# Performance work log

Hardware: AMD Instinct MI355X
Metric: run time of the kernel (lower is better)

## Reference

```python
import jax, jax.numpy as jnp
import numpy as np

DROPOUT_P = 0.1  # original source passed p=1 (degenerate, zeros output); 0.1 used for a meaningful baseline


def setup_inputs() -> dict:
    key0 = jax.random.key(0)
    ks = jax.random.split(key0, 11)
    B, H, L, D, DQK, DV = 2, 8, 2048, 1024, 64, 64
    return {
        "query": jax.random.normal(ks[0], (B, H, L, D), jnp.float32),
        "key":   jax.random.normal(ks[1], (B, H, L, D), jnp.float32),
        "value": jax.random.normal(ks[2], (B, H, L, D), jnp.float32),
        "Wq": jax.random.normal(ks[3], (D, DQK), jnp.float32) * (D ** -0.5),
        "bq": jax.random.normal(ks[4], (DQK,), jnp.float32) * 0.02,
        "Wk": jax.random.normal(ks[5], (D, DQK), jnp.float32) * (D ** -0.5),
        "bk": jax.random.normal(ks[6], (DQK,), jnp.float32) * 0.02,
        "Wv": jax.random.normal(ks[7], (D, DV), jnp.float32) * (D ** -0.5),
        "bv": jax.random.normal(ks[8], (DV,), jnp.float32) * 0.02,
        "Wo": jax.random.normal(ks[9], (DV, D), jnp.float32) * (DV ** -0.5),
        "bo": jax.random.normal(ks[10], (D,), jnp.float32) * 0.02,
    }


def reference(query, key, value, Wq, bq, Wk, bk, Wv, bv, Wo, bo):
    # Per-head linear projections on 4D inputs (B,H,L,d_model)
    q = query @ Wq + bq            # (B,H,Lq,dqk)
    k = key @ Wk + bk              # (B,H,Lk,dqk)
    v = value @ Wv + bv            # (B,H,Lk,dv)
    # Quirky scale from source: q.size(2)*q.size(3)/key.size(2) * key.size(-1)**-0.5
    dk = (q.shape[2] * q.shape[3] / key.shape[2]) * (key.shape[-1] ** -0.5)
    scores = jnp.einsum('bhqd,bhkd->bhqk', q, k) * jnp.float32(dk)
    attn = jax.nn.softmax(scores, axis=-1)
    # Deterministic dropout with fixed key (inverted-scale, matching F.dropout)
    keep = jax.random.bernoulli(jax.random.key(42), 1.0 - DROPOUT_P, attn.shape)
    attn = jnp.where(keep, attn / (1.0 - DROPOUT_P), jnp.float32(0.0))
    out = jnp.einsum('bhqk,bhkd->bhqd', attn, v)  # (B,H,Lq,dv)
    return out @ Wo + bo                           # (B,H,Lq,d_model)
```

## Files before the change

### kernel.cpp

```cpp
#include <hip/hip_runtime.h>
#include <stdint.h>

typedef _Float16 f16;
typedef __attribute__((ext_vector_type(8))) _Float16 f16x8;
typedef __attribute__((ext_vector_type(4))) float f32x4;

__device__ __forceinline__ uint32_t rotl1(uint32_t x, uint32_t n){
  return __builtin_amdgcn_alignbit(x, x, 32u - n);
}
__device__ __forceinline__ uint32_t tf_bits(uint32_t i){
  const uint32_t ks1 = 42u, ks2 = 0x1BD11BDAu ^ 42u;
  uint32_t x0 = 0u, x1 = i + 42u;
#define R4(a,b,c,d) \
  x0 += x1; x1 = rotl1(x1,a); x1 ^= x0; \
  x0 += x1; x1 = rotl1(x1,b); x1 ^= x0; \
  x0 += x1; x1 = rotl1(x1,c); x1 ^= x0; \
  x0 += x1; x1 = rotl1(x1,d); x1 ^= x0;
  R4(13,15,26,6)  x0 += ks1; x1 += ks2 + 1u;
  R4(17,29,16,24) x0 += ks2; x1 += 2u;
  R4(13,15,26,6)               x1 += ks1 + 3u;
  R4(17,29,16,24) x0 += ks1; x1 += ks2 + 4u;
  R4(13,15,26,6)  x0 += ks2; x1 += 5u;
#undef R4
  return x0 ^ x1;
}

template<int PACKED>
__global__ __launch_bounds__(256) void proj_kernel(
    const float* __restrict__ query, const float* __restrict__ keyp, const float* __restrict__ value,
    const float* __restrict__ Wq, const float* __restrict__ bq,
    const float* __restrict__ Wk, const float* __restrict__ bk,
    const float* __restrict__ Wv, const float* __restrict__ bv,
    const float* __restrict__ Wo,
    f16* __restrict__ qp, f16* __restrict__ kp, f16* __restrict__ vpT,
    f16* __restrict__ WoT)
{
  __shared__ __align__(16) f16 Alds[64][40];
  __shared__ __align__(16) f16 Wlds[64][40];
  const int bid = blockIdx.x;
  const int tid = threadIdx.x;
  const int lane = tid & 63, wave = tid >> 6;
  const int llo = lane & 15, lhi = lane >> 4;

  int p;
  if (PACKED == 0){
    if (bid < 256){
      int t = bid*256 + tid;
      int n = t & 1023, k = t >> 10;
      WoT[(long)n*64 + k] = (f16)Wo[(long)k*1024 + n];
      return;
    }
    p = bid - 256;
  } else {
    p = 768 + bid;
  }

  const int which = p >> 9;
  const long m0 = (long)(p & 511) * 64;
  const float* A    = which==0 ? query : (which==1 ? keyp : value);
  const float* W    = which==0 ? Wq    : (which==1 ? Wk   : Wv);
  const float* bias = which==0 ? bq    : (which==1 ? bk   : bv);

  f32x4 acc[4];
  #pragma unroll
  for (int n=0;n<4;n++){
    float bb = bias[16*n + llo];
    acc[n][0]=bb; acc[n][1]=bb; acc[n][2]=bb; acc[n][3]=bb;
  }

  const int ar = tid >> 2;
  const int ac = (tid & 3) * 8;
  const int wcol = tid & 63;
  const int wk = (tid >> 6) * 8;

  for (int k0 = 0; k0 < 1024; k0 += 32){
    {
      const float* asrc = A + (m0 + ar)*1024 + k0 + ac;
      float4 v0 = *(const float4*)asrc;
      float4 v1 = *(const float4*)(asrc + 4);
      if (PACKED == 0){
        f16* ad = &Alds[ar][ac];
        ad[0]=(f16)v0.x; ad[1]=(f16)v0.y; ad[2]=(f16)v0.z; ad[3]=(f16)v0.w;
        ad[4]=(f16)v1.x; ad[5]=(f16)v1.y; ad[6]=(f16)v1.z; ad[7]=(f16)v1.w;
      } else {
        union { f16 h[8]; f16x8 v; } aw;
        aw.h[0]=(f16)v0.x; aw.h[1]=(f16)v0.y; aw.h[2]=(f16)v0.z; aw.h[3]=(f16)v0.w;
        aw.h[4]=(f16)v1.x; aw.h[5]=(f16)v1.y; aw.h[6]=(f16)v1.z; aw.h[7]=(f16)v1.w;
        *(f16x8*)&Alds[ar][ac] = aw.v;
      }
      f16 wt[8];
      #pragma unroll
      for (int j=0;j<8;j++) wt[j] = (f16)W[(long)(k0+wk+j)*64 + wcol];
      *(f16x8*)&Wlds[wcol][wk] = *(f16x8*)wt;
    }
    __syncthreads();
    f16x8 af = *(const f16x8*)&Alds[wave*16 + llo][lhi*8];
    #pragma unroll
    for (int n=0;n<4;n++){
      f16x8 bf = *(const f16x8*)&Wlds[16*n + llo][lhi*8];
      acc[n] = __builtin_amdgcn_mfma_f32_16x16x32_f16(af, bf, acc[n], 0,0,0);
    }
    __syncthreads();
  }

  if (which < 2){
    const float scale = (which==0) ? 2.0f : 1.0f;
    f16* dst = (which==0) ? qp : kp;
    #pragma unroll
    for (int n=0;n<4;n++)
      #pragma unroll
      for (int j=0;j<4;j++){
        long row = m0 + wave*16 + lhi*4 + j;
        dst[row*64 + 16*n + llo] = (f16)(acc[n][j]*scale);
      }
  } else {
    long row0 = m0 + wave*16 + lhi*4;
    long bh = row0 >> 11;
    long lr = row0 & 2047;
    #pragma unroll
    for (int n=0;n<4;n++){
      union { f16 h[4]; ushort4 u; } pk;
      #pragma unroll
      for (int j=0;j<4;j++) pk.h[j] = (f16)acc[n][j];
      *(ushort4*)&vpT[(bh*64 + 16*n + llo)*2048 + lr] = pk.u;
    }
  }
}

__global__ __launch_bounds__(256) void flash_kernel(
    const f16* __restrict__ qp, const f16* __restrict__ kp, const f16* __restrict__ vpT,
    const f16* __restrict__ WoT, const float* __restrict__ bo, float* __restrict__ out)
{
  __shared__ __align__(16) f16 Klds[2][64][72];
  __shared__ __align__(16) f16 Vlds[2][64][72];
  __shared__ __align__(16) f16 Plds[4][16][72];
  __shared__ unsigned short Idl[4][1024];
  const int tid = threadIdx.x;
  const int lane = tid & 63, wave = tid >> 6;
  const int llo = lane & 15, lhi = lane >> 4;
  const int bh = blockIdx.y;
  const int q0 = blockIdx.x * 64;

  const f16* qbase = qp + ((long)bh*2048 + q0 + wave*16 + llo)*64 + lhi*8;
  f16x8 qf0 = *(const f16x8*)qbase;
  f16x8 qf1 = *(const f16x8*)(qbase + 32);

  f16x8 ones1;
  #pragma unroll
  for (int e=0;e<8;e++) ones1[e] = (f16)1.0f;

  f32x4 O[4];
  float mrun[4], lrun[4];
  #pragma unroll
  for (int n=0;n<4;n++){ O[n][0]=0.f;O[n][1]=0.f;O[n][2]=0.f;O[n][3]=0.f; }
  #pragma unroll
  for (int j=0;j<4;j++){ mrun[j] = -__builtin_inff(); lrun[j]=0.f; }

  const int sr = tid >> 2;
  const int sc = (tid & 3) * 16;
  const f16* ksrc = kp + (long)bh*2048*64 + (long)sr*64 + sc;
  const f16* vsrc = vpT + (long)bh*64*2048 + (long)sr*2048 + sc;
  uint32_t base_w = (uint32_t)((bh*2048 + q0 + wave*16)*2048);

  f16x8 kr0 = *(const f16x8*)(ksrc);
  f16x8 kr1 = *(const f16x8*)(ksrc + 8);
  f16x8 vr0 = *(const f16x8*)(vsrc);
  f16x8 vr1 = *(const f16x8*)(vsrc + 8);
  *(f16x8*)&Klds[0][sr][sc]   = kr0;
  *(f16x8*)&Klds[0][sr][sc+8] = kr1;
  *(f16x8*)&Vlds[0][sr][sc]   = vr0;
  *(f16x8*)&Vlds[0][sr][sc+8] = vr1;
  __syncthreads();

  for (int t = 0; t < 32; ++t, base_w += 64u){
    const int buf = t & 1;
    if (t < 31){
      const f16* ks = ksrc + (long)(t+1)*4096;
      kr0 = *(const f16x8*)ks;
      kr1 = *(const f16x8*)(ks + 8);
      const f16* vs = vsrc + (long)(t+1)*64;
      vr0 = *(const f16x8*)vs;
      vr1 = *(const f16x8*)(vs + 8);
    }

    f32x4 s[4];
    #pragma unroll
    for (int n=0;n<4;n++){ s[n][0]=0.f;s[n][1]=0.f;s[n][2]=0.f;s[n][3]=0.f; }
    #pragma unroll
    for (int n=0;n<4;n++){
      f16x8 kf0 = *(const f16x8*)&Klds[buf][16*n+llo][lhi*8];
      s[n] = __builtin_amdgcn_mfma_f32_16x16x32_f16(qf0, kf0, s[n], 0,0,0);
      f16x8 kf1 = *(const f16x8*)&Klds[buf][16*n+llo][32+lhi*8];
      s[n] = __builtin_amdgcn_mfma_f32_16x16x32_f16(qf1, kf1, s[n], 0,0,0);
    }
    float pmax[4];
    #pragma unroll
    for (int j=0;j<4;j++)
      pmax[j] = fmaxf(fmaxf(s[0][j],s[1][j]), fmaxf(s[2][j],s[3][j]));
    #pragma unroll
    for (int off=1; off<16; off<<=1){
      #pragma unroll
      for (int j=0;j<4;j++) pmax[j] = fmaxf(pmax[j], __shfl_xor(pmax[j], off));
    }
    float esc[4];
    #pragma unroll
    for (int j=0;j<4;j++){
      float mnew = fmaxf(mrun[j], pmax[j]);
      esc[j] = __expf(mrun[j] - mnew);
      mrun[j] = mnew;
    }
    float p[4][4];
    #pragma unroll
    for (int n=0;n<4;n++)
      #pragma unroll
      for (int j=0;j<4;j++)
        p[n][j] = __expf(s[n][j] - mrun[j]);
    #pragma unroll
    for (int n=0;n<4;n++)
      #pragma unroll
      for (int j=0;j<4;j++) O[n][j] *= esc[j];

    uint32_t cnt = 0;
    #pragma unroll
    for (int j=0;j<4;j++){
      #pragma unroll
      for (int n=0;n<4;n++){
        float pm = p[n][j]*(1.0f/0.9f);
        bool surv = pm > 0x1.0p-25f;
        Plds[wave][lhi*4+j][16*n+llo] = (f16)pm;
        unsigned long long mk = __ballot(surv);
        if (mk){
          uint32_t pre = __builtin_amdgcn_mbcnt_hi((uint32_t)(mk>>32),
                         __builtin_amdgcn_mbcnt_lo((uint32_t)mk, 0u));
          if (surv)
            Idl[wave][cnt + pre] = (unsigned short)((j<<8)|(n<<6)|lane);
          cnt += (uint32_t)__builtin_popcountll(mk);
        }
      }
    }

    {
      f16x8 la0 = *(const f16x8*)&Plds[wave][llo][lhi*8];
      f16x8 la1 = *(const f16x8*)&Plds[wave][llo][32+lhi*8];
      f32x4 lc; lc[0]=0.f; lc[1]=0.f; lc[2]=0.f; lc[3]=0.f;
      lc = __builtin_amdgcn_mfma_f32_16x16x32_f16(la0, ones1, lc, 0,0,0);
      lc = __builtin_amdgcn_mfma_f32_16x16x32_f16(la1, ones1, lc, 0,0,0);
      #pragma unroll
      for (int j=0;j<4;j++) lrun[j] = lrun[j]*esc[j] + 0.9f*lc[j];
    }

    for (uint32_t pb = 0; pb < cnt; pb += 64){
      uint32_t idx = pb + (uint32_t)lane;
      if (idx < cnt){
        uint32_t id = (uint32_t)Idl[wave][idx];
        uint32_t jj = (id>>8)&3u, nn = (id>>6)&3u, ln = id & 63u;
        uint32_t i = base_w + (ln>>4)*8192u + jj*2048u + nn*16u + (ln&15u);
        uint32_t bits = tf_bits(i);
        if (bits >= 0xE6666600u)
          Plds[wave][(ln>>4)*4+jj][16*nn+(ln&15u)] = (f16)0;
      }
    }

    f16x8 pa0 = *(const f16x8*)&Plds[wave][llo][lhi*8];
    f16x8 pa1 = *(const f16x8*)&Plds[wave][llo][32+lhi*8];
    #pragma unroll
    for (int n=0;n<4;n++){
      f16x8 vf0 = *(const f16x8*)&Vlds[buf][16*n+llo][lhi*8];
      O[n] = __builtin_amdgcn_mfma_f32_16x16x32_f16(pa0, vf0, O[n], 0,0,0);
      f16x8 vf1 = *(const f16x8*)&Vlds[buf][16*n+llo][32+lhi*8];
      O[n] = __builtin_amdgcn_mfma_f32_16x16x32_f16(pa1, vf1, O[n], 0,0,0);
    }

    if (t < 31){
      *(f16x8*)&Klds[buf^1][sr][sc]   = kr0;
      *(f16x8*)&Klds[buf^1][sr][sc+8] = kr1;
      *(f16x8*)&Vlds[buf^1][sr][sc]   = vr0;
      *(f16x8*)&Vlds[buf^1][sr][sc+8] = vr1;
    }
    __syncthreads();
  }

  float rl[4];
  #pragma unroll
  for (int j=0;j<4;j++) rl[j] = 1.0f / lrun[j];
  #pragma unroll
  for (int n=0;n<4;n++)
    #pragma unroll
    for (int j=0;j<4;j++)
      Klds[0][wave*16 + lhi*4 + j][16*n + llo] = (f16)(O[n][j]*rl[j]);
  __syncthreads();

  f16x8 af0 = *(const f16x8*)&Klds[0][wave*16 + llo][lhi*8];
  f16x8 af1 = *(const f16x8*)&Klds[0][wave*16 + llo][32 + lhi*8];
  const long robase = (long)bh*2048 + q0 + wave*16 + lhi*4;
  for (int n0 = 0; n0 < 1024; n0 += 16){
    f16x8 b0 = *(const f16x8*)&WoT[(long)(n0+llo)*64 + lhi*8];
    f16x8 b1 = *(const f16x8*)&WoT[(long)(n0+llo)*64 + 32 + lhi*8];
    float bb = bo[n0+llo];
    f32x4 c; c[0]=bb; c[1]=bb; c[2]=bb; c[3]=bb;
    c = __builtin_amdgcn_mfma_f32_16x16x32_f16(af0, b0, c, 0,0,0);
    c = __builtin_amdgcn_mfma_f32_16x16x32_f16(af1, b1, c, 0,0,0);
    #pragma unroll
    for (int j=0;j<4;j++)
      out[(robase + j)*1024 + n0 + llo] = c[j];
  }
}

extern "C" void kernel_launch(void* const* d_in, const int* in_sizes, int n_in,
                              void* d_out, int out_size, void* d_ws, size_t ws_size,
                              hipStream_t stream){
  const float* query = (const float*)d_in[0];
  const float* key   = (const float*)d_in[1];
  const float* value = (const float*)d_in[2];
  const float* Wq = (const float*)d_in[3];
  const float* bq = (const float*)d_in[4];
  const float* Wk = (const float*)d_in[5];
  const float* bk = (const float*)d_in[6];
  const float* Wv = (const float*)d_in[7];
  const float* bv = (const float*)d_in[8];
  const float* Wo = (const float*)d_in[9];
  const float* bo = (const float*)d_in[10];
  float* out = (float*)d_out;

  char* ws = (char*)d_ws;
  f16* qp   = (f16*)(ws);
  f16* kp   = (f16*)(ws + ((size_t)4<<20));
  f16* vpT  = (f16*)(ws + ((size_t)8<<20));
  f16* WoT  = (f16*)(ws + ((size_t)20<<20));

  proj_kernel<0><<<dim3(1024), dim3(256), 0, stream>>>(
      query,key,value,Wq,bq,Wk,bk,Wv,bv,Wo,qp,kp,vpT,WoT);
  proj_kernel<1><<<dim3(768), dim3(256), 0, stream>>>(
      query,key,value,Wq,bq,Wk,bk,Wv,bv,Wo,qp,kp,vpT,WoT);
  flash_kernel<<<dim3(32,16), dim3(256), 0, stream>>>(qp,kp,vpT,WoT,bo,out);
}
```

Measured before the change: 239.1 us.

## Merge projection launches, add lazy softmax rescaling, and use LDS atomics for survivor compaction

Merges the two projection launches into one 1792-block grid and reorders it so the Wo transpose blocks run last. The A-tile LDS stores go back to scalar f16 writes everywhere. In the flash kernel, the running max and the O/l rescale now update only when the new row max exceeds the old one by more than 8. This skips most exp and multiply work but lets unnormalised values grow up to e^8 in fp16 P. The ballot/mbcnt compaction of surviving dropout indices is replaced by per-wave LDS atomicAdd counters, which may serialize and make index order nondeterministic.

```diff
diff --git a/kernel.cpp b/kernel.cpp
--- a/kernel.cpp
+++ b/kernel.cpp
@@ -25,7 +25,6 @@
   return x0 ^ x1;
 }
 
-template<int PACKED>
 __global__ __launch_bounds__(256) void proj_kernel(
     const float* __restrict__ query, const float* __restrict__ keyp, const float* __restrict__ value,
     const float* __restrict__ Wq, const float* __restrict__ bq,
@@ -42,19 +41,13 @@
   const int lane = tid & 63, wave = tid >> 6;
   const int llo = lane & 15, lhi = lane >> 4;
 
-  int p;
-  if (PACKED == 0){
-    if (bid < 256){
-      int t = bid*256 + tid;
-      int n = t & 1023, k = t >> 10;
-      WoT[(long)n*64 + k] = (f16)Wo[(long)k*1024 + n];
-      return;
-    }
-    p = bid - 256;
-  } else {
-    p = 768 + bid;
-  }
-
+  if (bid >= 1536){
+    int t = (bid - 1536)*256 + tid;
+    int n = t & 1023, k = t >> 10;
+    WoT[(long)n*64 + k] = (f16)Wo[(long)k*1024 + n];
+    return;
+  }
+  const int p = bid;
   const int which = p >> 9;
   const long m0 = (long)(p & 511) * 64;
   const float* A    = which==0 ? query : (which==1 ? keyp : value);
@@ -78,16 +71,9 @@
       const float* asrc = A + (m0 + ar)*1024 + k0 + ac;
       float4 v0 = *(const float4*)asrc;
       float4 v1 = *(const float4*)(asrc + 4);
-      if (PACKED == 0){
-        f16* ad = &Alds[ar][ac];
-        ad[0]=(f16)v0.x; ad[1]=(f16)v0.y; ad[2]=(f16)v0.z; ad[3]=(f16)v0.w;
-        ad[4]=(f16)v1.x; ad[5]=(f16)v1.y; ad[6]=(f16)v1.z; ad[7]=(f16)v1.w;
-      } else {
-        union { f16 h[8]; f16x8 v; } aw;
-        aw.h[0]=(f16)v0.x; aw.h[1]=(f16)v0.y; aw.h[2]=(f16)v0.z; aw.h[3]=(f16)v0.w;
-        aw.h[4]=(f16)v1.x; aw.h[5]=(f16)v1.y; aw.h[6]=(f16)v1.z; aw.h[7]=(f16)v1.w;
-        *(f16x8*)&Alds[ar][ac] = aw.v;
-      }
+      f16* ad = &Alds[ar][ac];
+      ad[0]=(f16)v0.x; ad[1]=(f16)v0.y; ad[2]=(f16)v0.z; ad[3]=(f16)v0.w;
+      ad[4]=(f16)v1.x; ad[5]=(f16)v1.y; ad[6]=(f16)v1.z; ad[7]=(f16)v1.w;
       f16 wt[8];
       #pragma unroll
       for (int j=0;j<8;j++) wt[j] = (f16)W[(long)(k0+wk+j)*64 + wcol];
@@ -135,6 +121,7 @@
   __shared__ __align__(16) f16 Vlds[2][64][72];
   __shared__ __align__(16) f16 Plds[4][16][72];
   __shared__ unsigned short Idl[4][1024];
+  __shared__ uint32_t Cnt[4];
   const int tid = threadIdx.x;
   const int lane = tid & 63, wave = tid >> 6;
   const int llo = lane & 15, lhi = lane >> 4;
@@ -202,42 +189,46 @@
       #pragma unroll
       for (int j=0;j<4;j++) pmax[j] = fmaxf(pmax[j], __shfl_xor(pmax[j], off));
     }
-    float esc[4];
-    #pragma unroll
-    for (int j=0;j<4;j++){
-      float mnew = fmaxf(mrun[j], pmax[j]);
-      esc[j] = __expf(mrun[j] - mnew);
-      mrun[j] = mnew;
-    }
+
+    float adv = fmaxf(fmaxf(pmax[0]-mrun[0], pmax[1]-mrun[1]),
+                      fmaxf(pmax[2]-mrun[2], pmax[3]-mrun[3]));
+    if (adv > 8.0f){
+      float esc[4];
+      #pragma unroll
+      for (int j=0;j<4;j++){
+        float mnew = fmaxf(mrun[j], pmax[j]);
+        esc[j] = __expf(mrun[j] - mnew);
+        mrun[j] = mnew;
+      }
+      #pragma unroll
+      for (int j=0;j<4;j++) lrun[j] *= esc[j];
+      #pragma unroll
+      for (int n=0;n<4;n++)
+        #pragma unroll
+        for (int j=0;j<4;j++) O[n][j] *= esc[j];
+    }
+
     float p[4][4];
     #pragma unroll
     for (int n=0;n<4;n++)
       #pragma unroll
       for (int j=0;j<4;j++)
         p[n][j] = __expf(s[n][j] - mrun[j]);
-    #pragma unroll
-    for (int n=0;n<4;n++)
-      #pragma unroll
-      for (int j=0;j<4;j++) O[n][j] *= esc[j];
-
-    uint32_t cnt = 0;
+
+    if (lane == 0) Cnt[wave] = 0;
     #pragma unroll
     for (int j=0;j<4;j++){
       #pragma unroll
       for (int n=0;n<4;n++){
         float pm = p[n][j]*(1.0f/0.9f);
-        bool surv = pm > 0x1.0p-25f;
         Plds[wave][lhi*4+j][16*n+llo] = (f16)pm;
-        unsigned long long mk = __ballot(surv);
-        if (mk){
-          uint32_t pre = __builtin_amdgcn_mbcnt_hi((uint32_t)(mk>>32),
-                         __builtin_amdgcn_mbcnt_lo((uint32_t)mk, 0u));
-          if (surv)
-            Idl[wave][cnt + pre] = (unsigned short)((j<<8)|(n<<6)|lane);
-          cnt += (uint32_t)__builtin_popcountll(mk);
+        if (pm > 0x1.0p-25f){
+          uint32_t pos = atomicAdd(&Cnt[wave], 1u);
+          Idl[wave][pos] = (unsigned short)((j<<8)|(n<<6)|lane);
         }
       }
     }
+    uint32_t cnt = Cnt[wave];
 
     {
       f16x8 la0 = *(const f16x8*)&Plds[wave][llo][lhi*8];
@@ -246,7 +237,7 @@
       lc = __builtin_amdgcn_mfma_f32_16x16x32_f16(la0, ones1, lc, 0,0,0);
       lc = __builtin_amdgcn_mfma_f32_16x16x32_f16(la1, ones1, lc, 0,0,0);
       #pragma unroll
-      for (int j=0;j<4;j++) lrun[j] = lrun[j]*esc[j] + 0.9f*lc[j];
+      for (int j=0;j<4;j++) lrun[j] += 0.9f*lc[j];
     }
 
     for (uint32_t pb = 0; pb < cnt; pb += 64){
@@ -328,9 +319,7 @@
   f16* vpT  = (f16*)(ws + ((size_t)8<<20));
   f16* WoT  = (f16*)(ws + ((size_t)20<<20));
 
-  proj_kernel<0><<<dim3(1024), dim3(256), 0, stream>>>(
-      query,key,value,Wq,bq,Wk,bk,Wv,bv,Wo,qp,kp,vpT,WoT);
-  proj_kernel<1><<<dim3(768), dim3(256), 0, stream>>>(
+  proj_kernel<<<dim3(1792), dim3(256), 0, stream>>>(
       query,key,value,Wq,bq,Wk,bk,Wv,bv,Wo,qp,kp,vpT,WoT);
   flash_kernel<<<dim3(32,16), dim3(256), 0, stream>>>(qp,kp,vpT,WoT,bo,out);
 }
```

Result: slower. 249.0 us (+4.1%).
